# Kernel tuning notes

Hardware: AMD Instinct MI355X
Metric: run time of the kernel (lower is better)

The kernel has to match this reference:

```python
import jax, jax.numpy as jnp
import numpy as np

N_ATOMS = 50000
N_PAIRS = 1000000
F = 64   # per-atom features
G = 16   # radial basis functions
V = 32   # vector features
H1 = 128
IN_F = F + V + 1 + V  # 129, non-first interaction module
OUT_F = F + 2


def setup_inputs() -> dict:
    key = jax.random.key(0)
    ks = jax.random.split(key, 12)
    return {
        "atomic_embedding": jax.random.normal(ks[0], (N_ATOMS, F), dtype=jnp.float32),
        "partial_charges": jax.random.normal(ks[1], (N_ATOMS, 1), dtype=jnp.float32),
        "gs": jax.random.uniform(ks[2], (N_PAIRS, G), dtype=jnp.float32),
        "gv": jax.random.normal(ks[3], (N_PAIRS, 3, G), dtype=jnp.float32),
        "agh": jax.random.normal(ks[4], (F, G, V), dtype=jnp.float32) * (1.0 / np.sqrt(G)),
        "W1": jax.random.normal(ks[5], (IN_F, H1), dtype=jnp.float32) * (1.0 / np.sqrt(IN_F)),
        "b1": jnp.zeros((H1,), dtype=jnp.float32),
        "W2": jax.random.normal(ks[6], (H1, H1), dtype=jnp.float32) * (1.0 / np.sqrt(H1)),
        "b2": jnp.zeros((H1,), dtype=jnp.float32),
        "W3": jax.random.normal(ks[7], (H1, OUT_F), dtype=jnp.float32) * (1.0 / np.sqrt(H1)),
        "b3": jnp.zeros((OUT_F,), dtype=jnp.float32),
        "pair_indices": jax.random.randint(ks[8], (2, N_PAIRS), 0, N_ATOMS, dtype=jnp.int64),
    }


def _interaction(atomic_embedding, partial_charges, gs, gv, agh,
                 W1, b1, W2, b2, W3, b3, idx_j):
    n_atoms = atomic_embedding.shape[0]
    v = agh.shape[-1]

    # --- embedding branch ---
    a_j = atomic_embedding[idx_j]                      # (P, F) gather
    # torch: (gs[:,:,None] * a_j[:,None,:]).sum(1) == gs.sum(1, keepdims) * a_j
    avf_s = jnp.einsum('pg,pf->pf', gs, a_j)           # (P, F)
    radial_emb = jax.ops.segment_sum(avf_s, idx_j, num_segments=n_atoms)  # (N, F)

    avf_v = jnp.einsum('pa,pdg,agh->phd', a_j, gv, agh)  # (P, V, 3)
    vec_emb = jax.ops.segment_sum(jnp.sum(avf_v * avf_v, axis=-1),
                                  idx_j, num_segments=n_atoms)            # (N, V)

    # --- partial-charge branch (agh=None path) ---
    q_j = partial_charges[idx_j]                       # (P, 1)
    avf_s_q = jnp.einsum('pg,pf->pf', gs, q_j)         # (P, 1)
    radial_q = jax.ops.segment_sum(avf_s_q, idx_j, num_segments=n_atoms)  # (N, 1)
    vec_q = jnp.zeros((n_atoms, v), dtype=atomic_embedding.dtype)         # (N, V)

    msg = jnp.concatenate([radial_emb, vec_emb, radial_q, vec_q], axis=1)  # (N, F+V+1+V)

    h = jax.nn.gelu(msg @ W1 + b1, approximate=False)
    h = jax.nn.gelu(h @ W2 + b2, approximate=False)
    out = h @ W3 + b3                                   # (N, F+2)

    delta_q = out[:, 0:1]
    f = out[:, 1:2]
    delta_a = out[:, 2:]
    return delta_a, delta_q, f


def reference(atomic_embedding, partial_charges, gs, gv, agh,
              W1, b1, W2, b2, W3, b3, pair_indices):
    idx_j = pair_indices[1]
    return _interaction(atomic_embedding, partial_charges, gs, gv, agh,
                        W1, b1, W2, b2, W3, b3, idx_j)
```

## Files before the change

### kernel.cpp

```cpp
#include <hip/hip_runtime.h>
#include <math.h>

#define NA 50000
#define NP 1000000
#define OUTF 66
#define SCAN_BLOCKS 196


__global__ void k_hist(const int* __restrict__ idxj, int* __restrict__ cnt) {
    int p = blockIdx.x * 256 + threadIdx.x;
    if (p < NP) atomicAdd(&cnt[idxj[p]], 1);
}

__global__ __launch_bounds__(256) void k_scanA(const int* __restrict__ cnt,
                                               int* __restrict__ blkS) {
    __shared__ int sh[256];
    int t = threadIdx.x;
    int i = blockIdx.x * 256 + t;
    sh[t] = (i < NA) ? cnt[i] : 0;
    __syncthreads();
    for (int d = 128; d > 0; d >>= 1) {
        if (t < d) sh[t] += sh[t + d];
        __syncthreads();
    }
    if (t == 0) blkS[blockIdx.x] = sh[0];
}

__global__ __launch_bounds__(256) void k_scanB(int* __restrict__ blkS) {
    __shared__ int sh[256];
    int t = threadIdx.x;
    sh[t] = (t < SCAN_BLOCKS) ? blkS[t] : 0;
    __syncthreads();
    for (int d = 1; d < 256; d <<= 1) {
        int x = (t >= d) ? sh[t - d] : 0;
        __syncthreads();
        sh[t] += x;
        __syncthreads();
    }
    int e = (t == 0) ? 0 : sh[t - 1];
    if (t < SCAN_BLOCKS) blkS[t] = e;
}

__global__ __launch_bounds__(256) void k_scanC(const int* __restrict__ cnt,
                                               const int* __restrict__ blkS,
                                               int* __restrict__ offs,
                                               int* __restrict__ curs) {
    __shared__ int sh[256];
    int t = threadIdx.x;
    int i = blockIdx.x * 256 + t;
    sh[t] = (i < NA) ? cnt[i] : 0;
    __syncthreads();
    for (int d = 1; d < 256; d <<= 1) {
        int x = (t >= d) ? sh[t - d] : 0;
        __syncthreads();
        sh[t] += x;
        __syncthreads();
    }
    int excl = ((t == 0) ? 0 : sh[t - 1]) + blkS[blockIdx.x];
    if (i < NA) { offs[i] = excl; curs[i] = excl; }
}

__global__ void k_scatter(const int* __restrict__ idxj, int* __restrict__ curs,
                          int* __restrict__ sortedP) {
    int p = blockIdx.x * 256 + threadIdx.x;
    if (p < NP) {
        int i = idxj[p];
        int pos = atomicAdd(&curs[i], 1);
        sortedP[pos] = (p << 3) | (i & 7);
    }
}

__global__ __launch_bounds__(256) void k_atoms(const float* __restrict__ emb,
                                               const float* __restrict__ agh,
                                               const float* __restrict__ gs,
                                               const float* __restrict__ gv,
                                               const int* __restrict__ sortedP,
                                               const int* __restrict__ offs,
                                               float* __restrict__ S,
                                               float* __restrict__ vec) {
    __shared__ float embS[8][64];
    __shared__ float T_lds[8][32][20];
    __shared__ float vecS[8][32];
    __shared__ float sS[8];
    const int t = threadIdx.x;
    const int atom0 = blockIdx.x * 8;

    vecS[t >> 5][t & 31] = 0.f;
    if (t < 8) sS[t] = 0.f;
    for (int k = t; k < 8 * 64; k += 256)
        embS[k >> 6][k & 63] = emb[(size_t)atom0 * 64 + k];
    __syncthreads();

    {
        float acc0[8], acc1[8];
#pragma unroll
        for (int at = 0; at < 8; ++at) { acc0[at] = 0.f; acc1[at] = 0.f; }
        const int gh0 = t, gh1 = t + 256;
        for (int a = 0; a < 64; ++a) {
            float w0 = agh[a * 512 + gh0];
            float w1 = agh[a * 512 + gh1];
#pragma unroll
            for (int at = 0; at < 8; ++at) {
                float e = embS[at][a];
                acc0[at] += e * w0;
                acc1[at] += e * w1;
            }
        }
        const int g0 = gh0 >> 5, h0 = gh0 & 31;
        const int g1 = gh1 >> 5, h1 = gh1 & 31;
#pragma unroll
        for (int at = 0; at < 8; ++at) {
            T_lds[at][h0][g0] = acc0[at];
            T_lds[at][h1][g1] = acc1[at];
        }
    }
    __syncthreads();

    const int wv = t >> 6, lane = t & 63;
    const int pr = lane >> 2, q = lane & 3;
    const int hb = q * 8;
    const int start = offs[atom0];
    const int end = (atom0 + 8 < NA) ? offs[atom0 + 8] : NP;

    for (int k0 = start + wv * 16; k0 < end; k0 += 64) {
        const int k = k0 + pr;
        const bool ok = k < end;
        int pk = ok ? sortedP[k] : 0;
        const int p = pk >> 3, at = pk & 7;

        float gq = 0.f;
        if (ok) {
            float4 g4 = ((const float4*)gs)[(size_t)p * 4 + q];
            gq = (g4.x + g4.y) + (g4.z + g4.w);
        }
        gq += __shfl_xor(gq, 1);
        gq += __shfl_xor(gq, 2);
        if (ok && q == 0) atomicAdd(&sS[at], gq);

        if (ok) {
            float gvr[48];
            const float4* gv4 = (const float4*)(gv + (size_t)p * 48);
#pragma unroll
            for (int j = 0; j < 12; ++j) ((float4*)gvr)[j] = gv4[j];

#pragma unroll
            for (int hh = 0; hh < 8; ++hh) {
                const float4* Tr = (const float4*)&T_lds[at][hb + hh][0];
                float4 t0 = Tr[0], t1 = Tr[1], t2 = Tr[2], t3 = Tr[3];
                float Trow[16] = {t0.x, t0.y, t0.z, t0.w, t1.x, t1.y, t1.z, t1.w,
                                  t2.x, t2.y, t2.z, t2.w, t3.x, t3.y, t3.z, t3.w};
                float v0 = 0.f, v1 = 0.f, v2 = 0.f;
#pragma unroll
                for (int g = 0; g < 16; ++g) {
                    float tg = Trow[g];
                    v0 += gvr[g] * tg;
                    v1 += gvr[16 + g] * tg;
                    v2 += gvr[32 + g] * tg;
                }
                atomicAdd(&vecS[at][hb + hh], v0 * v0 + v1 * v1 + v2 * v2);
            }
        }
    }
    __syncthreads();

    vec[(size_t)(atom0 + (t >> 5)) * 32 + (t & 31)] = vecS[t >> 5][t & 31];
    if (t < 8) S[atom0 + t] = sS[t];
}

#define MSTR 132
__global__ __launch_bounds__(256) void k_mlp(const float* __restrict__ emb,
                                             const float* __restrict__ q,
                                             const float* __restrict__ S,
                                             const float* __restrict__ vec,
                                             const float* __restrict__ W1,
                                             const float* __restrict__ b1,
                                             const float* __restrict__ W2,
                                             const float* __restrict__ b2,
                                             const float* __restrict__ W3,
                                             const float* __restrict__ b3,
                                             float* __restrict__ out) {
    __shared__ float bufA[64 * MSTR];
    __shared__ float bufB[64 * MSTR];
    const int t = threadIdx.x;
    const int atom0 = blockIdx.x * 64;

    for (int k = t; k < 64 * 97; k += 256) {
        int a = k / 97, c = k - a * 97;
        int i = atom0 + a;
        float val = 0.f;
        if (i < NA) {
            float s = S[i];
            if (c < 64) val = emb[(size_t)i * 64 + c] * s;
            else if (c < 96) val = vec[(size_t)i * 32 + (c - 64)];
            else val = q[i] * s;
        }
        bufA[a * MSTR + c] = val;
    }
    __syncthreads();

    const int jg = t & 31, ag = t >> 5;
    const int j0 = 4 * jg;
    const int abase = ag * 8;
    float acc[8][4];

    {
        float4 bb = *(const float4*)&b1[j0];
#pragma unroll
        for (int a = 0; a < 8; ++a) {
            acc[a][0] = bb.x; acc[a][1] = bb.y; acc[a][2] = bb.z; acc[a][3] = bb.w;
        }
        for (int k4 = 0; k4 < 96; k4 += 4) {
            float4 w0 = *(const float4*)&W1[(k4 + 0) * 128 + j0];
            float4 w1 = *(const float4*)&W1[(k4 + 1) * 128 + j0];
            float4 w2 = *(const float4*)&W1[(k4 + 2) * 128 + j0];
            float4 w3 = *(const float4*)&W1[(k4 + 3) * 128 + j0];
#pragma unroll
            for (int a = 0; a < 8; ++a) {
                float4 m = *(const float4*)&bufA[(abase + a) * MSTR + k4];
                acc[a][0] += m.x * w0.x + m.y * w1.x + m.z * w2.x + m.w * w3.x;
                acc[a][1] += m.x * w0.y + m.y * w1.y + m.z * w2.y + m.w * w3.y;
                acc[a][2] += m.x * w0.z + m.y * w1.z + m.z * w2.z + m.w * w3.z;
                acc[a][3] += m.x * w0.w + m.y * w1.w + m.z * w2.w + m.w * w3.w;
            }
        }
        {
            float4 w = *(const float4*)&W1[96 * 128 + j0];
#pragma unroll
            for (int a = 0; a < 8; ++a) {
                float m = bufA[(abase + a) * MSTR + 96];
                acc[a][0] += m * w.x; acc[a][1] += m * w.y;
                acc[a][2] += m * w.z; acc[a][3] += m * w.w;
            }
        }
#pragma unroll
        for (int a = 0; a < 8; ++a) {
            float4 o;
            o.x = 0.5f * acc[a][0] * (1.f + erff(acc[a][0] * 0.70710678118654752f));
            o.y = 0.5f * acc[a][1] * (1.f + erff(acc[a][1] * 0.70710678118654752f));
            o.z = 0.5f * acc[a][2] * (1.f + erff(acc[a][2] * 0.70710678118654752f));
            o.w = 0.5f * acc[a][3] * (1.f + erff(acc[a][3] * 0.70710678118654752f));
            *(float4*)&bufB[(abase + a) * MSTR + j0] = o;
        }
    }
    __syncthreads();

    {
        float4 bb = *(const float4*)&b2[j0];
#pragma unroll
        for (int a = 0; a < 8; ++a) {
            acc[a][0] = bb.x; acc[a][1] = bb.y; acc[a][2] = bb.z; acc[a][3] = bb.w;
        }
        for (int k4 = 0; k4 < 128; k4 += 4) {
            float4 w0 = *(const float4*)&W2[(k4 + 0) * 128 + j0];
            float4 w1 = *(const float4*)&W2[(k4 + 1) * 128 + j0];
            float4 w2 = *(const float4*)&W2[(k4 + 2) * 128 + j0];
            float4 w3 = *(const float4*)&W2[(k4 + 3) * 128 + j0];
#pragma unroll
            for (int a = 0; a < 8; ++a) {
                float4 m = *(const float4*)&bufB[(abase + a) * MSTR + k4];
                acc[a][0] += m.x * w0.x + m.y * w1.x + m.z * w2.x + m.w * w3.x;
                acc[a][1] += m.x * w0.y + m.y * w1.y + m.z * w2.y + m.w * w3.y;
                acc[a][2] += m.x * w0.z + m.y * w1.z + m.z * w2.z + m.w * w3.z;
                acc[a][3] += m.x * w0.w + m.y * w1.w + m.z * w2.w + m.w * w3.w;
            }
        }
#pragma unroll
        for (int a = 0; a < 8; ++a) {
            float4 o;
            o.x = 0.5f * acc[a][0] * (1.f + erff(acc[a][0] * 0.70710678118654752f));
            o.y = 0.5f * acc[a][1] * (1.f + erff(acc[a][1] * 0.70710678118654752f));
            o.z = 0.5f * acc[a][2] * (1.f + erff(acc[a][2] * 0.70710678118654752f));
            o.w = 0.5f * acc[a][3] * (1.f + erff(acc[a][3] * 0.70710678118654752f));
            *(float4*)&bufA[(abase + a) * MSTR + j0] = o;
        }
    }
    __syncthreads();

    if (j0 < OUTF) {
#pragma unroll
        for (int a = 0; a < 8; ++a) {
            acc[a][0] = b3[j0];
            acc[a][1] = (j0 + 1 < OUTF) ? b3[j0 + 1] : 0.f;
            acc[a][2] = (j0 + 2 < OUTF) ? b3[j0 + 2] : 0.f;
            acc[a][3] = (j0 + 3 < OUTF) ? b3[j0 + 3] : 0.f;
        }
        for (int k = 0; k < 128; ++k) {
            float w0 = W3[k * OUTF + j0];
            float w1 = (j0 + 1 < OUTF) ? W3[k * OUTF + j0 + 1] : 0.f;
            float w2 = (j0 + 2 < OUTF) ? W3[k * OUTF + j0 + 2] : 0.f;
            float w3 = (j0 + 3 < OUTF) ? W3[k * OUTF + j0 + 3] : 0.f;
#pragma unroll
            for (int a = 0; a < 8; ++a) {
                float m = bufA[(abase + a) * MSTR + k];
                acc[a][0] += m * w0; acc[a][1] += m * w1;
                acc[a][2] += m * w2; acc[a][3] += m * w3;
            }
        }
#pragma unroll
        for (int a = 0; a < 8; ++a) {
            int i = atom0 + abase + a;
            if (i < NA) {
#pragma unroll
                for (int c = 0; c < 4; ++c) {
                    int j = j0 + c;
                    if (j < OUTF) {
                        if (j == 0)
                            out[(size_t)NA * 64 + i] = acc[a][c];
                        else if (j == 1)
                            out[(size_t)NA * 64 + NA + i] = acc[a][c];
                        else
                            out[(size_t)i * 64 + (j - 2)] = acc[a][c];
                    }
                }
            }
        }
    }
}

extern "C" void kernel_launch(void* const* d_in, const int* in_sizes, int n_in,
                              void* d_out, int out_size, void* d_ws, size_t ws_size,
                              hipStream_t stream) {
    const float* emb = (const float*)d_in[0];
    const float* q   = (const float*)d_in[1];
    const float* gs  = (const float*)d_in[2];
    const float* gv  = (const float*)d_in[3];
    const float* agh = (const float*)d_in[4];
    const float* W1  = (const float*)d_in[5];
    const float* b1  = (const float*)d_in[6];
    const float* W2  = (const float*)d_in[7];
    const float* b2  = (const float*)d_in[8];
    const float* W3  = (const float*)d_in[9];
    const float* b3  = (const float*)d_in[10];
    const int* pairs = (const int*)d_in[11];
    const int* idxj  = pairs + NP;

    int*   cnt     = (int*)d_ws;
    int*   offs    = cnt + NA;
    int*   curs    = offs + NA;
    int*   blkS    = curs + NA;
    int*   sortedP = blkS + 256;
    float* S       = (float*)(sortedP + NP);
    float* vec     = S + NA;

    hipMemsetAsync(cnt, 0, NA * sizeof(int), stream);
    k_hist<<<(NP + 255) / 256, 256, 0, stream>>>(idxj, cnt);
    k_scanA<<<SCAN_BLOCKS, 256, 0, stream>>>(cnt, blkS);
    k_scanB<<<1, 256, 0, stream>>>(blkS);
    k_scanC<<<SCAN_BLOCKS, 256, 0, stream>>>(cnt, blkS, offs, curs);
    k_scatter<<<(NP + 255) / 256, 256, 0, stream>>>(idxj, curs, sortedP);
    k_atoms<<<NA / 8, 256, 0, stream>>>(emb, agh, gs, gv, sortedP, offs, S, vec);
    k_mlp<<<(NA + 63) / 64, 256, 0, stream>>>(emb, q, S, vec,
                                              W1, b1, W2, b2, W3, b3,
                                              (float*)d_out);
}
```

Measured before the change: 806.1 us.

## Process one pair per thread over 16-atom blocks with pairwise-combined LDS atomics

The atom-block kernel now covers 16 atoms per block instead of 8, and the pair index packs a 4-bit local atom id. Each thread handles a whole pair and computes all 32 vector channels itself, instead of four lanes splitting a pair eight channels each. Neighbouring lanes that share an atom combine their values through a shuffle before the shared-memory atomic, roughly halving atomic traffic. The trade-off is higher register pressure from 48 gv values plus accumulators, and a different load pattern for gs and gv.

```diff
diff --git a/kernel.cpp b/kernel.cpp
--- a/kernel.cpp
+++ b/kernel.cpp
@@ -5,6 +5,8 @@
 #define NP 1000000
 #define OUTF 66
 #define SCAN_BLOCKS 196
+#define ATB 16
+#define TSTR 516
 
 
 __global__ void k_hist(const int* __restrict__ idxj, int* __restrict__ cnt) {
@@ -66,7 +68,7 @@
     if (p < NP) {
         int i = idxj[p];
         int pos = atomicAdd(&curs[i], 1);
-        sortedP[pos] = (p << 3) | (i & 7);
+        sortedP[pos] = (p << 4) | (i & 15);
     }
 }
 
@@ -78,93 +80,107 @@
                                                const int* __restrict__ offs,
                                                float* __restrict__ S,
                                                float* __restrict__ vec) {
-    __shared__ float embS[8][64];
-    __shared__ float T_lds[8][32][20];
-    __shared__ float vecS[8][32];
-    __shared__ float sS[8];
+    __shared__ float T_lds[ATB * TSTR];
+    __shared__ float embS[ATB * 64];
+    __shared__ float vecS[ATB * 33];
+    __shared__ float sS[ATB];
     const int t = threadIdx.x;
-    const int atom0 = blockIdx.x * 8;
-
-    vecS[t >> 5][t & 31] = 0.f;
-    if (t < 8) sS[t] = 0.f;
-    for (int k = t; k < 8 * 64; k += 256)
-        embS[k >> 6][k & 63] = emb[(size_t)atom0 * 64 + k];
+    const int atom0 = blockIdx.x * ATB;
+
+    for (int k = t; k < ATB * 33; k += 256) vecS[k] = 0.f;
+    if (t < ATB) sS[t] = 0.f;
+    for (int k = t; k < ATB * 64; k += 256) embS[k] = emb[(size_t)atom0 * 64 + k];
     __syncthreads();
 
     {
-        float acc0[8], acc1[8];
-#pragma unroll
-        for (int at = 0; at < 8; ++at) { acc0[at] = 0.f; acc1[at] = 0.f; }
-        const int gh0 = t, gh1 = t + 256;
+        float acc0[ATB], acc1[ATB];
+#pragma unroll
+        for (int at = 0; at < ATB; ++at) { acc0[at] = 0.f; acc1[at] = 0.f; }
+        const int c0 = t, c1 = t + 256;
         for (int a = 0; a < 64; ++a) {
-            float w0 = agh[a * 512 + gh0];
-            float w1 = agh[a * 512 + gh1];
-#pragma unroll
-            for (int at = 0; at < 8; ++at) {
-                float e = embS[at][a];
+            float w0 = agh[a * 512 + c0];
+            float w1 = agh[a * 512 + c1];
+#pragma unroll
+            for (int at = 0; at < ATB; ++at) {
+                float e = embS[at * 64 + a];
                 acc0[at] += e * w0;
                 acc1[at] += e * w1;
             }
         }
-        const int g0 = gh0 >> 5, h0 = gh0 & 31;
-        const int g1 = gh1 >> 5, h1 = gh1 & 31;
-#pragma unroll
-        for (int at = 0; at < 8; ++at) {
-            T_lds[at][h0][g0] = acc0[at];
-            T_lds[at][h1][g1] = acc1[at];
-        }
-    }
-    __syncthreads();
-
-    const int wv = t >> 6, lane = t & 63;
-    const int pr = lane >> 2, q = lane & 3;
-    const int hb = q * 8;
+        const int g0 = c0 >> 5, h0 = c0 & 31;
+        const int g1 = c1 >> 5, h1 = c1 & 31;
+#pragma unroll
+        for (int at = 0; at < ATB; ++at) {
+            T_lds[at * TSTR + h0 * 16 + g0] = acc0[at];
+            T_lds[at * TSTR + h1 * 16 + g1] = acc1[at];
+        }
+    }
+    __syncthreads();
+
+    const int lane = t & 63;
     const int start = offs[atom0];
-    const int end = (atom0 + 8 < NA) ? offs[atom0 + 8] : NP;
-
-    for (int k0 = start + wv * 16; k0 < end; k0 += 64) {
-        const int k = k0 + pr;
-        const bool ok = k < end;
-        int pk = ok ? sortedP[k] : 0;
-        const int p = pk >> 3, at = pk & 7;
-
-        float gq = 0.f;
-        if (ok) {
-            float4 g4 = ((const float4*)gs)[(size_t)p * 4 + q];
-            gq = (g4.x + g4.y) + (g4.z + g4.w);
-        }
-        gq += __shfl_xor(gq, 1);
-        gq += __shfl_xor(gq, 2);
-        if (ok && q == 0) atomicAdd(&sS[at], gq);
-
-        if (ok) {
-            float gvr[48];
-            const float4* gv4 = (const float4*)(gv + (size_t)p * 48);
-#pragma unroll
-            for (int j = 0; j < 12; ++j) ((float4*)gvr)[j] = gv4[j];
-
-#pragma unroll
-            for (int hh = 0; hh < 8; ++hh) {
-                const float4* Tr = (const float4*)&T_lds[at][hb + hh][0];
-                float4 t0 = Tr[0], t1 = Tr[1], t2 = Tr[2], t3 = Tr[3];
-                float Trow[16] = {t0.x, t0.y, t0.z, t0.w, t1.x, t1.y, t1.z, t1.w,
-                                  t2.x, t2.y, t2.z, t2.w, t3.x, t3.y, t3.z, t3.w};
-                float v0 = 0.f, v1 = 0.f, v2 = 0.f;
-#pragma unroll
-                for (int g = 0; g < 16; ++g) {
-                    float tg = Trow[g];
-                    v0 += gvr[g] * tg;
-                    v1 += gvr[16 + g] * tg;
-                    v2 += gvr[32 + g] * tg;
-                }
-                atomicAdd(&vecS[at][hb + hh], v0 * v0 + v1 * v1 + v2 * v2);
-            }
-        }
-    }
-    __syncthreads();
-
-    vec[(size_t)(atom0 + (t >> 5)) * 32 + (t & 31)] = vecS[t >> 5][t & 31];
-    if (t < 8) S[atom0 + t] = sS[t];
+    const int end = (blockIdx.x + 1 < 3125) ? offs[atom0 + ATB] : NP;
+
+    for (int kb = start; kb < end; kb += 256) {
+        const int k = kb + t;
+        const bool ok = (k < end);
+        const int pk = ok ? sortedP[k] : 0;
+        const int p = ok ? (pk >> 4) : 0;
+        const int at = pk & 15;
+        const int atm = ok ? at : (64 + lane);
+
+        const int atn = __shfl_xor(atm, 1);
+        const bool same = (atn == atm);
+        const bool flush = (!same) || ((lane & 1) == 0);
+
+        float gvr[48];
+        const float4* gv4 = (const float4*)(gv + (size_t)p * 48);
+#pragma unroll
+        for (int j = 0; j < 12; ++j) ((float4*)gvr)[j] = gv4[j];
+
+        const float4* gs4 = (const float4*)(gs + (size_t)p * 16);
+        float4 ga = gs4[0], gb = gs4[1], gc = gs4[2], gd = gs4[3];
+        float gq = (ga.x + ga.y + ga.z + ga.w) + (gb.x + gb.y + gb.z + gb.w) +
+                   (gc.x + gc.y + gc.z + gc.w) + (gd.x + gd.y + gd.z + gd.w);
+        float gqn = __shfl_xor(gq, 1);
+        float gqm = gq + (same ? gqn : 0.f);
+        if (ok && flush) atomicAdd(&sS[at], gqm);
+
+        const float* Tb = &T_lds[at * TSTR];
+#pragma unroll 4
+        for (int h = 0; h < 32; ++h) {
+            const float4* Tr = (const float4*)(Tb + h * 16);
+            float4 t0 = Tr[0], t1 = Tr[1], t2 = Tr[2], t3 = Tr[3];
+            float v0, v1, v2;
+            v0  = gvr[0]  * t0.x; v1  = gvr[16] * t0.x; v2  = gvr[32] * t0.x;
+            v0 += gvr[1]  * t0.y; v1 += gvr[17] * t0.y; v2 += gvr[33] * t0.y;
+            v0 += gvr[2]  * t0.z; v1 += gvr[18] * t0.z; v2 += gvr[34] * t0.z;
+            v0 += gvr[3]  * t0.w; v1 += gvr[19] * t0.w; v2 += gvr[35] * t0.w;
+            v0 += gvr[4]  * t1.x; v1 += gvr[20] * t1.x; v2 += gvr[36] * t1.x;
+            v0 += gvr[5]  * t1.y; v1 += gvr[21] * t1.y; v2 += gvr[37] * t1.y;
+            v0 += gvr[6]  * t1.z; v1 += gvr[22] * t1.z; v2 += gvr[38] * t1.z;
+            v0 += gvr[7]  * t1.w; v1 += gvr[23] * t1.w; v2 += gvr[39] * t1.w;
+            v0 += gvr[8]  * t2.x; v1 += gvr[24] * t2.x; v2 += gvr[40] * t2.x;
+            v0 += gvr[9]  * t2.y; v1 += gvr[25] * t2.y; v2 += gvr[41] * t2.y;
+            v0 += gvr[10] * t2.z; v1 += gvr[26] * t2.z; v2 += gvr[42] * t2.z;
+            v0 += gvr[11] * t2.w; v1 += gvr[27] * t2.w; v2 += gvr[43] * t2.w;
+            v0 += gvr[12] * t3.x; v1 += gvr[28] * t3.x; v2 += gvr[44] * t3.x;
+            v0 += gvr[13] * t3.y; v1 += gvr[29] * t3.y; v2 += gvr[45] * t3.y;
+            v0 += gvr[14] * t3.z; v1 += gvr[30] * t3.z; v2 += gvr[46] * t3.z;
+            v0 += gvr[15] * t3.w; v1 += gvr[31] * t3.w; v2 += gvr[47] * t3.w;
+            float e = v0 * v0 + v1 * v1 + v2 * v2;
+            float en = __shfl_xor(e, 1);
+            float em = e + (same ? en : 0.f);
+            if (ok && flush) atomicAdd(&vecS[at * 33 + h], em);
+        }
+    }
+    __syncthreads();
+
+    for (int k = t; k < ATB * 32; k += 256) {
+        int a = k >> 5, h = k & 31;
+        vec[(size_t)(atom0 + a) * 32 + h] = vecS[a * 33 + h];
+    }
+    if (t < ATB) S[atom0 + t] = sS[t];
 }
 
 #define MSTR 132
@@ -348,7 +364,7 @@
     k_scanB<<<1, 256, 0, stream>>>(blkS);
     k_scanC<<<SCAN_BLOCKS, 256, 0, stream>>>(cnt, blkS, offs, curs);
     k_scatter<<<(NP + 255) / 256, 256, 0, stream>>>(idxj, curs, sortedP);
-    k_atoms<<<NA / 8, 256, 0, stream>>>(emb, agh, gs, gv, sortedP, offs, S, vec);
+    k_atoms<<<NA / ATB, 256, 0, stream>>>(emb, agh, gs, gv, sortedP, offs, S, vec);
     k_mlp<<<(NA + 63) / 64, 256, 0, stream>>>(emb, q, S, vec,
                                               W1, b1, W2, b2, W3, b3,
                                               (float*)d_out);
```

After: 785.7 us. 1.03x faster.
